# Performance work log

Hardware: AMD Instinct MI355X
Metric: run time of the kernel (lower is better)

The kernel has to match this reference:

```python
import jax, jax.numpy as jnp
import numpy as np

B, S, D, H, E = 4, 1024, 1024, 16, 4
HD = D // H
EPS = 1e-5


def setup_inputs() -> dict:
    key = jax.random.key(0)
    ks = jax.random.split(key, 6)
    std = 0.02
    return {
        "hidden_states": jax.random.normal(ks[0], (B, S, D), dtype=jnp.float32),
        "Wr": jax.random.normal(ks[1], (D, E), dtype=jnp.float32) * std,
        "br": jnp.zeros((E,), jnp.float32),
        "ln_g": jnp.ones((E, D), jnp.float32),
        "ln_b": jnp.zeros((E, D), jnp.float32),
        "W_attn": jax.random.normal(ks[2], (E, D, 3 * D), dtype=jnp.float32) * std,
        "b_attn": jnp.zeros((E, 3 * D), jnp.float32),
        "W_proj": jax.random.normal(ks[3], (E, D, D), dtype=jnp.float32) * std,
        "b_proj": jnp.zeros((E, D), jnp.float32),
    }


def reference(hidden_states, Wr, br, ln_g, ln_b, W_attn, b_attn, W_proj, b_proj):
    b, s, d = hidden_states.shape
    x = hidden_states.reshape(b * s, d)  # [N, D]

    # naive softmax router over experts
    score = jax.nn.softmax(x @ Wr + br, axis=-1)  # [N, E]

    # LayerNorm stats are expert-independent; affine is per-expert
    mu = jnp.mean(x, axis=-1, keepdims=True)
    var = jnp.mean(jnp.square(x - mu), axis=-1, keepdims=True)
    xn = (x - mu) * jax.lax.rsqrt(var + EPS)  # [N, D]

    ln_out = xn[:, None, :] * ln_g[None] + ln_b[None]  # [N, E, D]
    qkv_all = jnp.einsum('ned,edf->nef', ln_out, W_attn) + b_attn  # [N, E, 3D]
    # weighted_qkv: scale each expert's qkv by its routing score, sum
    qkv = jnp.einsum('ne,nef->nf', score, qkv_all)  # [N, 3D]

    q, k, v = jnp.split(qkv.reshape(b, s, 3 * d), 3, axis=-1)
    def split_heads(t):
        return t.reshape(b, s, H, HD).transpose(0, 2, 1, 3)  # [B,H,S,hd]
    q, k, v = split_heads(q), split_heads(k), split_heads(v)

    scale = 1.0 / jnp.sqrt(jnp.asarray(HD, q.dtype))
    att = jnp.einsum('bhqd,bhkd->bhqk', q, k) * scale  # [B,H,S,S]
    causal = jnp.tril(jnp.ones((s, s), dtype=bool))
    att = jnp.where(causal[None, None], att, jnp.finfo(att.dtype).min)
    probs = jax.nn.softmax(att, axis=-1)
    ctx = jnp.einsum('bhqk,bhkd->bhqd', probs, v)  # [B,H,S,hd]
    ctx = ctx.transpose(0, 2, 1, 3).reshape(b * s, d)  # [N, D]

    proj_all = jnp.einsum('nd,edf->nef', ctx, W_proj) + b_proj  # [N, E, D]
    out = jnp.einsum('ne,nef->nf', score, proj_all).reshape(b, s, d)
    return out
```

## Files before the change

kernel.cpp:

```cpp
#include <hip/hip_runtime.h>
#include <stdint.h>

#define NB 4
#define SS 1024
#define DD 1024
#define EE 4
#define HH 16
#define HDD 64
#define NN (NB*SS)
#define KK2 (EE*DD)
#define FF1 (3*DD)

typedef __attribute__((ext_vector_type(4))) float f32x4;
typedef __attribute__((ext_vector_type(8))) _Float16 half8;
typedef __attribute__((ext_vector_type(4))) _Float16 half4;

static __device__ __forceinline__ f32x4 mfma16(half8 a, half8 b, f32x4 c){
  return __builtin_amdgcn_mfma_f32_16x16x32_f16(a, b, c, 0, 0, 0);
}

#define GLOAD_LDS16(gp, lp) __builtin_amdgcn_global_load_lds( \
    (const unsigned int __attribute__((address_space(1)))*)(uintptr_t)(gp), \
    (unsigned int __attribute__((address_space(3)))*)(uintptr_t)(lp), 16, 0, 0)

#define SBAR() do { asm volatile("" ::: "memory"); \
                    __builtin_amdgcn_s_barrier(); \
                    asm volatile("" ::: "memory"); } while(0)

__global__ __launch_bounds__(256) void prep_kernel(
    const float* __restrict__ x, const float* __restrict__ Wr,
    const float* __restrict__ br, float* __restrict__ score,
    float* __restrict__ ratios, _Float16* __restrict__ xnb)
{
  int n = blockIdx.x;
  int tid = threadIdx.x;
  float4 xv = ((const float4*)(x + (size_t)n*DD))[tid];
  float xa[4] = {xv.x, xv.y, xv.z, xv.w};
  float vals[6];
  vals[0] = xa[0]+xa[1]+xa[2]+xa[3];
  vals[1] = xa[0]*xa[0]+xa[1]*xa[1]+xa[2]*xa[2]+xa[3]*xa[3];
  vals[2] = vals[3] = vals[4] = vals[5] = 0.f;
  #pragma unroll
  for (int j = 0; j < 4; ++j){
    float4 w = ((const float4*)Wr)[tid*4 + j];
    vals[2] += xa[j]*w.x; vals[3] += xa[j]*w.y;
    vals[4] += xa[j]*w.z; vals[5] += xa[j]*w.w;
  }
  #pragma unroll
  for (int off = 32; off >= 1; off >>= 1)
    #pragma unroll
    for (int i = 0; i < 6; ++i)
      vals[i] += __shfl_xor(vals[i], off, 64);
  __shared__ float red[4][6];
  int wid = tid >> 6;
  if ((tid & 63) == 0){
    #pragma unroll
    for (int i = 0; i < 6; ++i) red[wid][i] = vals[i];
  }
  __syncthreads();
  float tot[6];
  #pragma unroll
  for (int i = 0; i < 6; ++i)
    tot[i] = red[0][i] + red[1][i] + red[2][i] + red[3][i];

  float mu   = tot[0] * (1.f/DD);
  float var  = tot[1] * (1.f/DD) - mu*mu;
  float rsig = rsqrtf(var + 1e-5f);
  float lg[4];
  #pragma unroll
  for (int e = 0; e < 4; ++e) lg[e] = tot[2+e] + br[e];
  float mx = fmaxf(fmaxf(lg[0], lg[1]), fmaxf(lg[2], lg[3]));
  float ex[4], esum = 0.f;
  #pragma unroll
  for (int e = 0; e < 4; ++e){ ex[e] = __expf(lg[e] - mx); esum += ex[e]; }
  if (tid < 4){
    score[n*4 + tid] = ex[tid] / esum;
    ratios[n*4 + tid] = (tid > 0) ? (ex[tid-1] / ex[tid]) : 0.f;
  }

  half4 o;
  #pragma unroll
  for (int j = 0; j < 4; ++j) o[j] = (_Float16)((xa[j] - mu) * rsig);
  *(half4*)(xnb + (size_t)n*DD + tid*4) = o;
}

template<bool AFFINE>
__global__ __launch_bounds__(256) void transpose_f16_kernel(
    const float* __restrict__ W, _Float16* __restrict__ WT, int K, int F,
    const float* __restrict__ gvec, const float* __restrict__ bvec,
    float* __restrict__ part)
{
  __shared__ float t[64][65];
  __shared__ float red2[16][64];
  int k0 = blockIdx.x * 64, f0 = blockIdx.y * 64;
  int tid = threadIdx.x;
  int r = tid >> 4, c4 = (tid & 15) * 4;
  float pf[4] = {0.f, 0.f, 0.f, 0.f};
  #pragma unroll
  for (int i = 0; i < 4; ++i){
    int k = k0 + i*16 + r;
    float4 v = *(const float4*)(W + (size_t)k*F + f0 + c4);
    if constexpr (AFFINE){
      float bk = bvec[k];
      pf[0] += bk*v.x; pf[1] += bk*v.y; pf[2] += bk*v.z; pf[3] += bk*v.w;
      float gk = gvec[k];
      v.x *= gk; v.y *= gk; v.z *= gk; v.w *= gk;
    }
    t[i*16 + r][c4+0] = v.x; t[i*16 + r][c4+1] = v.y;
    t[i*16 + r][c4+2] = v.z; t[i*16 + r][c4+3] = v.w;
  }
  if constexpr (AFFINE){
    #pragma unroll
    for (int j = 0; j < 4; ++j) red2[r][c4+j] = pf[j];
  }
  __syncthreads();
  int f = tid >> 2, seg = tid & 3;
  half8 o0, o1;
  #pragma unroll
  for (int j = 0; j < 8; ++j){
    o0[j] = (_Float16)t[seg*16 + j][f];
    o1[j] = (_Float16)t[seg*16 + 8 + j][f];
  }
  _Float16* dst = WT + (size_t)(f0 + f)*K + k0 + seg*16;
  *(half8*)dst = o0;
  *(half8*)(dst + 8) = o1;
  if constexpr (AFFINE){
    if (tid < 64){
      float s = 0.f;
      #pragma unroll
      for (int rr = 0; rr < 16; ++rr) s += red2[rr][tid];
      part[(size_t)blockIdx.x * F + f0 + tid] = s;
    }
  }
}

__global__ __launch_bounds__(256) void bb1_kernel(
    const float* __restrict__ b_attn, const float* __restrict__ part,
    float* __restrict__ BB1)
{
  int idx = blockIdx.x*256 + threadIdx.x;
  int e = idx / FF1, f = idx - e*FF1;
  float s = b_attn[idx];
  #pragma unroll
  for (int i = 0; i < 16; ++i)
    s += part[(size_t)(e*16 + i)*FF1 + f];
  BB1[idx] = s;
}

#define G1_BM 256
#define G1_BN 192
#define G1_BK 64
#define G1_T  (KK2/G1_BK)
#define G1_ABUF (G1_BM*G1_BK)
#define G1_BBUF (G1_BN*G1_BK)
#define G1_BUFSZ (G1_ABUF+G1_BBUF)

__global__ __launch_bounds__(512, 2) void gemm1_kernel(
    const _Float16* __restrict__ XN, const _Float16* __restrict__ BT,
    const float* __restrict__ score, const float* __restrict__ ratios,
    const float* __restrict__ bias, _Float16* __restrict__ C)
{
  __shared__ _Float16 smem[2*G1_BUFSZ];
  int tid = threadIdx.x;
  int lane = tid & 63, wid = tid >> 6;
  int q = lane & 15, g = lane >> 4;
  int wr = wid >> 1, wc = wid & 1;
  int xo = (q & 7) << 3;
  int bid = blockIdx.x;
  int xcd = bid & 7, li = bid >> 3;
  int m0 = (li >> 1) * G1_BM;
  int n0 = (xcd*2 + (li & 1)) * G1_BN;

  int arow[4], brow[6];
  #pragma unroll
  for (int mf = 0; mf < 4; ++mf) arow[mf] = (wr*64 + mf*16 + q)*64;
  #pragma unroll
  for (int nf = 0; nf < 6; ++nf) brow[nf] = G1_ABUF + (wc*96 + nf*16 + q)*64;
  int soff[2] = { (g*8) ^ xo, (32 + g*8) ^ xo };

  auto stageA = [&](int t, int buf, int h){
    const int d0 = (t & 15) * G1_BK;
    _Float16* sA = smem + buf*G1_BUFSZ;
    #pragma unroll
    for (int ld = 0; ld < 2; ++ld){
      int l = h*2 + ld;
      int c = l*512 + tid;
      int row = c >> 3;
      int seg = (c & 7) ^ (row & 7);
      GLOAD_LDS16(XN + (size_t)(m0 + row)*DD + d0 + seg*8,
                  sA + (l*512 + wid*64)*8);
    }
  };
  auto stageB = [&](int t, int buf){
    const int k0 = t * G1_BK;
    _Float16* sB = smem + buf*G1_BUFSZ + G1_ABUF;
    #pragma unroll
    for (int ld = 0; ld < 3; ++ld){
      int c = ld*512 + tid;
      int row = c >> 3;
      int seg = (c & 7) ^ (row & 7);
      GLOAD_LDS16(BT + (size_t)(n0 + row)*KK2 + k0 + seg*8,
                  sB + (ld*512 + wid*64)*8);
    }
  };

  f32x4 acc[4][6] = {};
  half8 af0[2][2], af2[2][2], bfA[3][2], bfB[3][2];

  auto C1 = [&](){
    __builtin_amdgcn_s_setprio(1);
    #pragma unroll
    for (int k = 0; k < 2; ++k)
      #pragma unroll
      for (int m = 0; m < 2; ++m)
        #pragma unroll
        for (int n = 0; n < 3; ++n)
          acc[m][n] = mfma16(af0[m][k], bfA[n][k], acc[m][n]);
    __builtin_amdgcn_s_setprio(0);
  };
  auto C2 = [&](){
    __builtin_amdgcn_s_setprio(1);
    #pragma unroll
    for (int k = 0; k < 2; ++k)
      #pragma unroll
      for (int m = 0; m < 2; ++m)
        #pragma unroll
        for (int n = 0; n < 3; ++n)
          acc[2+m][n] = mfma16(af2[m][k], bfA[n][k], acc[2+m][n]);
    __builtin_amdgcn_s_setprio(0);
  };
  auto C3 = [&](){
    __builtin_amdgcn_s_setprio(1);
    #pragma unroll
    for (int k = 0; k < 2; ++k)
      #pragma unroll
      for (int m = 0; m < 2; ++m)
        #pragma unroll
        for (int n = 0; n < 3; ++n)
          acc[m][3+n] = mfma16(af0[m][k], bfB[n][k], acc[m][3+n]);
    __builtin_amdgcn_s_setprio(0);
  };
  auto C4 = [&](){
    __builtin_amdgcn_s_setprio(1);
    #pragma unroll
    for (int k = 0; k < 2; ++k)
      #pragma unroll
      for (int m = 0; m < 2; ++m)
        #pragma unroll
        for (int n = 0; n < 3; ++n)
          acc[2+m][3+n] = mfma16(af2[m][k], bfB[n][k], acc[2+m][3+n]);
    __builtin_amdgcn_s_setprio(0);
  };

  stageA(0, 0, 0); stageA(0, 0, 1); stageB(0, 0);

  for (int t = 0; t < G1_T-1; ++t){
    int buf = t & 1, nxt = buf ^ 1;
    const _Float16* base = smem + buf*G1_BUFSZ;
    stageA(t+1, nxt, 0);
    asm volatile("s_waitcnt vmcnt(2)" ::: "memory");
    SBAR();
    #pragma unroll
    for (int m = 0; m < 2; ++m)
      #pragma unroll
      for (int k = 0; k < 2; ++k)
        af0[m][k] = *(const half8*)(base + arow[m] + soff[k]);
    #pragma unroll
    for (int n = 0; n < 3; ++n)
      #pragma unroll
      for (int k = 0; k < 2; ++k)
        bfA[n][k] = *(const half8*)(base + brow[n] + soff[k]);
    if (t) C4();
    if (t && (t & 15) == 0){
      int e = t >> 4;
      #pragma unroll
      for (int mf = 0; mf < 4; ++mf)
        #pragma unroll
        for (int r = 0; r < 4; ++r){
          int gm = m0 + wr*64 + mf*16 + g*4 + r;
          float ratio = ratios[gm*4 + e];
          #pragma unroll
          for (int nf = 0; nf < 6; ++nf)
            acc[mf][nf][r] *= ratio;
        }
    }
    C1();
    stageA(t+1, nxt, 1);
    #pragma unroll
    for (int m = 0; m < 2; ++m)
      #pragma unroll
      for (int k = 0; k < 2; ++k)
        af2[m][k] = *(const half8*)(base + arow[2+m] + soff[k]);
    C2();
    stageB(t+1, nxt);
    #pragma unroll
    for (int n = 0; n < 3; ++n)
      #pragma unroll
      for (int k = 0; k < 2; ++k)
        bfB[n][k] = *(const half8*)(base + brow[3+n] + soff[k]);
    SBAR();
    C3();
  }
  {
    const _Float16* base = smem + ((G1_T-1) & 1)*G1_BUFSZ;
    asm volatile("s_waitcnt vmcnt(0)" ::: "memory");
    SBAR();
    C4();
    #pragma unroll
    for (int m = 0; m < 2; ++m)
      #pragma unroll
      for (int k = 0; k < 2; ++k){
        af0[m][k] = *(const half8*)(base + arow[m] + soff[k]);
        af2[m][k] = *(const half8*)(base + arow[2+m] + soff[k]);
      }
    #pragma unroll
    for (int n = 0; n < 3; ++n)
      #pragma unroll
      for (int k = 0; k < 2; ++k){
        bfA[n][k] = *(const half8*)(base + brow[n] + soff[k]);
        bfB[n][k] = *(const half8*)(base + brow[3+n] + soff[k]);
      }
    C1(); C2(); C3(); C4();
  }

  float bv[6][4];
  #pragma unroll
  for (int nf = 0; nf < 6; ++nf){
    int gn = n0 + wc*96 + nf*16 + q;
    #pragma unroll
    for (int e = 0; e < 4; ++e) bv[nf][e] = bias[e*FF1 + gn];
  }
  #pragma unroll
  for (int mf = 0; mf < 4; ++mf){
    #pragma unroll
    for (int r = 0; r < 4; ++r){
      int gm = m0 + wr*64 + mf*16 + g*4 + r;
      float4 sc = *(const float4*)(score + gm*4);
      #pragma unroll
      for (int nf = 0; nf < 6; ++nf){
        int gn = n0 + wc*96 + nf*16 + q;
        float v = acc[mf][nf][r]*sc.w
                + sc.x*bv[nf][0] + sc.y*bv[nf][1] + sc.z*bv[nf][2] + sc.w*bv[nf][3];
        C[(size_t)gm*FF1 + gn] = (_Float16)v;
      }
    }
  }
}

#define G2_BK 64
#define G2_ABUF (128*G2_BK)
#define G2_BUFSZ (2*G2_ABUF)

__global__ __launch_bounds__(512) void gemm2_kernel(
    const _Float16* __restrict__ CTX, const _Float16* __restrict__ BT,
    const float* __restrict__ score, const float* __restrict__ bias,
    float* __restrict__ Cout)
{
  __shared__ _Float16 smem[2*G2_BUFSZ];
  int tid = threadIdx.x;
  int lane = tid & 63, wid = tid >> 6;
  int q = lane & 15, g = lane >> 4;
  int wr = wid >> 2, wc = wid & 3;
  int xo = (q & 7) << 3;
  int bid = blockIdx.x;
  int xcd = bid >> 5, idx = bid & 31;
  int m0 = (xcd*4 + (idx >> 3)) * 128;
  int n0 = (idx & 7) * 128;

  int arow[4], brow[2];
  #pragma unroll
  for (int mf = 0; mf < 4; ++mf) arow[mf] = (wr*64 + mf*16 + q)*64;
  #pragma unroll
  for (int nf = 0; nf < 2; ++nf) brow[nf] = G2_ABUF + (wc*32 + nf*16 + q)*64;
  int soff[2] = { (g*8) ^ xo, (32 + g*8) ^ xo };

  auto stage = [&](int t, int buf){
    const int d0 = (t & 15) * G2_BK;
    const int k0 = t * G2_BK;
    _Float16* sA = smem + buf*G2_BUFSZ;
    _Float16* sB = sA + G2_ABUF;
    #pragma unroll
    for (int ld = 0; ld < 2; ++ld){
      int c = ld*512 + tid;
      int row = c >> 3;
      int seg = (c & 7) ^ (row & 7);
      GLOAD_LDS16(CTX + (size_t)(m0 + row)*DD + d0 + seg*8,
                  sA + (ld*512 + wid*64)*8);
    }
    #pragma unroll
    for (int ld = 0; ld < 2; ++ld){
      int c = ld*512 + tid;
      int row = c >> 3;
      int seg = (c & 7) ^ (row & 7);
      GLOAD_LDS16(BT + (size_t)(n0 + row)*KK2 + k0 + seg*8,
                  sB + (ld*512 + wid*64)*8);
    }
  };

  f32x4 accp[4][2] = {}, acco[4][2] = {};

  auto merge = [&](int e){
    #pragma unroll
    for (int m = 0; m < 4; ++m)
      #pragma unroll
      for (int r = 0; r < 4; ++r){
        int gm = m0 + wr*64 + m*16 + g*4 + r;
        float s = score[(size_t)gm*4 + e];
        #pragma unroll
        for (int n = 0; n < 2; ++n){
          acco[m][n][r] += s*accp[m][n][r];
          accp[m][n][r] = 0.f;
        }
      }
  };

  half8 af[4][2], bfr[2][2];
  auto reads = [&](const _Float16* base, int k){
    #pragma unroll
    for (int m = 0; m < 4; ++m)
      af[m][k] = *(const half8*)(base + arow[m] + soff[k]);
    #pragma unroll
    for (int n = 0; n < 2; ++n)
      bfr[n][k] = *(const half8*)(base + brow[n] + soff[k]);
  };
  auto mfmas = [&](int k){
    __builtin_amdgcn_s_setprio(1);
    #pragma unroll
    for (int m = 0; m < 4; ++m)
      #pragma unroll
      for (int n = 0; n < 2; ++n)
        accp[m][n] = mfma16(af[m][k], bfr[n][k], accp[m][n]);
    __builtin_amdgcn_s_setprio(0);
  };

  stage(0, 0);
  for (int t = 0; t < KK2/G2_BK - 1; ++t){
    const _Float16* base = smem + (t & 1)*G2_BUFSZ;
    stage(t+1, (t+1)&1);
    asm volatile("s_waitcnt vmcnt(4)" ::: "memory");
    SBAR();
    reads(base, 0);
    if (t) mfmas(1);
    if (t && (t & 15) == 0) merge((t >> 4) - 1);
    mfmas(0);
    reads(base, 1);
    SBAR();
  }
  {
    const _Float16* base = smem + ((KK2/G2_BK - 1) & 1)*G2_BUFSZ;
    asm volatile("s_waitcnt vmcnt(0)" ::: "memory");
    SBAR();
    mfmas(1);
    reads(base, 0); reads(base, 1);
    mfmas(0); mfmas(1);
    merge(3);
  }

  #pragma unroll
  for (int m = 0; m < 4; ++m){
    #pragma unroll
    for (int r = 0; r < 4; ++r){
      int gm = m0 + wr*64 + m*16 + g*4 + r;
      float4 sc = *(const float4*)(score + gm*4);
      #pragma unroll
      for (int n = 0; n < 2; ++n){
        int gn = n0 + wc*32 + n*16 + q;
        float v = acco[m][n][r]
                + sc.x*bias[gn] + sc.y*bias[DD+gn]
                + sc.z*bias[2*DD+gn] + sc.w*bias[3*DD+gn];
        Cout[(size_t)gm*DD + gn] = v;
      }
    }
  }
}

__global__ __launch_bounds__(512) void attn_kernel(
    const _Float16* __restrict__ qkv, _Float16* __restrict__ ctx)
{
  __shared__ _Float16 lsK[2][64*64];
  __shared__ _Float16 lsV[2][64*64];
  __shared__ _Float16 lsP[8][16*64];
  int bh = blockIdx.x, qt = blockIdx.y;
  int b = bh >> 4, h = bh & 15;
  int tid = threadIdx.x, lane = tid & 63, wid = tid >> 6;
  int q = lane & 15, g = lane >> 4;
  int xo = (q & 7) << 3;
  int qrow0 = qt*128 + wid*16;

  half8 qf[2];
  #pragma unroll
  for (int kk = 0; kk < 2; ++kk)
    qf[kk] = *(const half8*)(qkv + ((size_t)b*SS + qrow0 + q)*FF1 + h*HDD + kk*32 + g*8);

  auto issueK = [&](int kt, int buf){
    size_t kvrow = (size_t)b*SS + kt*64;
    int row = tid >> 3, seg = (tid & 7) ^ (row & 7);
    GLOAD_LDS16(qkv + (kvrow + row)*FF1 + DD + h*HDD + seg*8,
                lsK[buf] + (size_t)(wid*64)*8);
  };
  auto issueV = [&](int kt, half8& vr){
    size_t kvrow = (size_t)b*SS + kt*64;
    vr = *(const half8*)(qkv + (kvrow + lane)*FF1 + 2*DD + h*HDD + wid*8);
  };
  auto writeV = [&](half8 vr, int buf){
    #pragma unroll
    for (int j = 0; j < 8; ++j){
      int hd = wid*8 + j;
      lsV[buf][hd*64 + (lane ^ ((hd & 7) << 3))] = vr[j];
    }
  };

  f32x4 o[4] = {};
  float mrow = -1e30f, lsum = 0.f;
  const float SC2 = 0.18033688011112042f;
  int qglob = qrow0 + q;
  int ktmax = 2*qt + 1;

  half8 vr;
  issueK(0, 0);
  issueV(0, vr);

  for (int kt = 0; kt <= ktmax; ++kt){
    int cur = kt & 1, nxt = cur ^ 1;
    int tn = (kt < ktmax) ? kt+1 : ktmax;
    asm volatile("s_waitcnt vmcnt(1)" ::: "memory");
    SBAR();

    f32x4 st[4] = {};
    __builtin_amdgcn_s_setprio(1);
    #pragma unroll
    for (int i = 0; i < 4; ++i){
      #pragma unroll
      for (int kk = 0; kk < 2; ++kk){
        half8 kf = *(const half8*)(lsK[cur] + (i*16 + q)*64 + ((kk*32 + g*8) ^ xo));
        st[i] = mfma16(kf, qf[kk], st[i]);
      }
    }
    __builtin_amdgcn_s_setprio(0);
    issueK(tn, nxt);
    asm volatile("s_waitcnt vmcnt(1)" ::: "memory");
    writeV(vr, cur);

    float pvv[16]; float tm = -1e30f;
    if (kt*64 + 63 > qrow0){
      #pragma unroll
      for (int i = 0; i < 4; ++i)
        #pragma unroll
        for (int r = 0; r < 4; ++r){
          int kglob = kt*64 + i*16 + g*4 + r;
          float sv = (kglob <= qglob) ? st[i][r]*SC2 : -1e30f;
          pvv[i*4+r] = sv; tm = fmaxf(tm, sv);
        }
    } else {
      #pragma unroll
      for (int i = 0; i < 4; ++i)
        #pragma unroll
        for (int r = 0; r < 4; ++r){
          float sv = st[i][r]*SC2;
          pvv[i*4+r] = sv; tm = fmaxf(tm, sv);
        }
    }
    tm = fmaxf(tm, __shfl_xor(tm, 16, 64));
    tm = fmaxf(tm, __shfl_xor(tm, 32, 64));
    bool resc = !__all(tm <= mrow);
    float mnew = resc ? fmaxf(mrow, tm) : mrow;
    float psum = 0.f;
    _Float16 pb[16];
    #pragma unroll
    for (int i = 0; i < 16; ++i){
      float p = exp2f(pvv[i] - mnew);
      psum += p; pb[i] = (_Float16)p;
    }
    if (resc){
      float alpha = exp2f(mrow - mnew);
      mrow = mnew;
      lsum = lsum*alpha + psum;
      float af4[4];
      #pragma unroll
      for (int r = 0; r < 4; ++r) af4[r] = __shfl(alpha, g*4 + r, 64);
      #pragma unroll
      for (int n = 0; n < 4; ++n)
        #pragma unroll
        for (int r = 0; r < 4; ++r) o[n][r] *= af4[r];
    } else {
      lsum += psum;
    }
    issueV(tn, vr);

    asm volatile("s_waitcnt lgkmcnt(0)" ::: "memory");
    SBAR();

    #pragma unroll
    for (int i = 0; i < 4; ++i){
      half4 w4;
      w4[0]=pb[i*4+0]; w4[1]=pb[i*4+1]; w4[2]=pb[i*4+2]; w4[3]=pb[i*4+3];
      *(half4*)(&lsP[wid][q*64 + ((i*16 + g*4) ^ xo)]) = w4;
    }
    __builtin_amdgcn_s_setprio(1);
    #pragma unroll
    for (int kk = 0; kk < 2; ++kk){
      half8 pf = *(const half8*)(&lsP[wid][q*64 + ((kk*32 + g*8) ^ xo)]);
      #pragma unroll
      for (int n = 0; n < 4; ++n){
        half8 vf = *(const half8*)(&lsV[cur][(n*16 + q)*64 + ((kk*32 + g*8) ^ xo)]);
        o[n] = mfma16(pf, vf, o[n]);
      }
    }
    __builtin_amdgcn_s_setprio(0);
  }
  float lt = lsum + __shfl_xor(lsum, 16, 64);
  lt = lt + __shfl_xor(lt, 32, 64);
  float rinv = 1.f / lt;
  #pragma unroll
  for (int r = 0; r < 4; ++r){
    float ri = __shfl(rinv, g*4 + r, 64);
    int qg = qt*128 + wid*16 + g*4 + r;
    _Float16* obase = ctx + ((size_t)b*SS + qg)*DD + h*HDD;
    #pragma unroll
    for (int n = 0; n < 4; ++n)
      obase[n*16 + q] = (_Float16)(o[n][r] * ri);
  }
}

extern "C" void kernel_launch(void* const* d_in, const int* in_sizes, int n_in,
                              void* d_out, int out_size, void* d_ws, size_t ws_size,
                              hipStream_t stream)
{
  const float* x      = (const float*)d_in[0];
  const float* Wr     = (const float*)d_in[1];
  const float* br     = (const float*)d_in[2];
  const float* ln_g   = (const float*)d_in[3];
  const float* ln_b   = (const float*)d_in[4];
  const float* W_attn = (const float*)d_in[5];
  const float* b_attn = (const float*)d_in[6];
  const float* W_proj = (const float*)d_in[7];
  const float* b_proj = (const float*)d_in[8];
  (void)in_sizes; (void)n_in; (void)out_size; (void)ws_size;

  char* ws = (char*)d_ws;
  size_t off = 0;
  auto alloc = [&](size_t bytes) -> void* {
    void* p = ws + off; off += (bytes + 255) & ~(size_t)255; return p;
  };
  _Float16* W1gT  = (_Float16*)alloc((size_t)FF1*KK2*2);
  _Float16* W2T   = (_Float16*)alloc((size_t)DD*KK2*2);
  float*    score = (float*)   alloc((size_t)NN*4*4);
  float*    ratio = (float*)   alloc((size_t)NN*4*4);
  _Float16* xn16  = (_Float16*)alloc((size_t)NN*DD*2);
  _Float16* qkv   = (_Float16*)alloc((size_t)NN*FF1*2);
  _Float16* ctx   = (_Float16*)alloc((size_t)NN*DD*2);
  float*    part  = (float*)   alloc((size_t)(KK2/64)*FF1*4);
  float*    BB1   = (float*)   alloc((size_t)EE*FF1*4);

  hipLaunchKernelGGL((transpose_f16_kernel<true>), dim3(KK2/64, FF1/64), dim3(256), 0, stream,
                     W_attn, W1gT, KK2, FF1, ln_g, ln_b, part);
  hipLaunchKernelGGL((transpose_f16_kernel<false>), dim3(KK2/64, DD/64), dim3(256), 0, stream,
                     W_proj, W2T, KK2, DD, nullptr, nullptr, nullptr);
  hipLaunchKernelGGL(bb1_kernel, dim3(EE*FF1/256), dim3(256), 0, stream,
                     b_attn, part, BB1);
  hipLaunchKernelGGL(prep_kernel, dim3(NN), dim3(256), 0, stream,
                     x, Wr, br, score, ratio, xn16);
  hipLaunchKernelGGL(gemm1_kernel, dim3(256), dim3(512), 0, stream,
                     xn16, W1gT, score, ratio, BB1, qkv);
  hipLaunchKernelGGL(attn_kernel, dim3(NB*HH, SS/128), dim3(512), 0, stream,
                     qkv, ctx);
  hipLaunchKernelGGL(gemm2_kernel, dim3(256), dim3(512), 0, stream,
                     ctx, W2T, score, b_proj, (float*)d_out);
}
```

Before: 200.7 us.

## Load GEMM1 A operand directly from global into registers, stage only B in LDS

The A operand (normalized activations) of the first GEMM is no longer staged through LDS; each wave loads its MFMA fragments directly from global memory into registers, double-buffered across iterations. LDS now holds only the B tiles, and the block-to-tile mapping is swapped so M follows the XCD index. The aim is to cut LDS footprint and LDS traffic for A, which is reused across the four experts' K-slices. In exchange, each wave issues uncoalesced 16-byte global loads per row, and the wait becomes a full vmcnt(0) with a simpler, less interleaved MFMA schedule.

```diff
diff --git a/kernel.cpp b/kernel.cpp
--- a/kernel.cpp
+++ b/kernel.cpp
@@ -151,16 +151,14 @@
 #define G1_BN 192
 #define G1_BK 64
 #define G1_T  (KK2/G1_BK)
-#define G1_ABUF (G1_BM*G1_BK)
 #define G1_BBUF (G1_BN*G1_BK)
-#define G1_BUFSZ (G1_ABUF+G1_BBUF)
 
 __global__ __launch_bounds__(512, 2) void gemm1_kernel(
     const _Float16* __restrict__ XN, const _Float16* __restrict__ BT,
     const float* __restrict__ score, const float* __restrict__ ratios,
     const float* __restrict__ bias, _Float16* __restrict__ C)
 {
-  __shared__ _Float16 smem[2*G1_BUFSZ];
+  __shared__ _Float16 smem[2*G1_BBUF];
   int tid = threadIdx.x;
   int lane = tid & 63, wid = tid >> 6;
   int q = lane & 15, g = lane >> 4;
@@ -168,32 +166,22 @@
   int xo = (q & 7) << 3;
   int bid = blockIdx.x;
   int xcd = bid & 7, li = bid >> 3;
-  int m0 = (li >> 1) * G1_BM;
-  int n0 = (xcd*2 + (li & 1)) * G1_BN;
-
-  int arow[4], brow[6];
-  #pragma unroll
-  for (int mf = 0; mf < 4; ++mf) arow[mf] = (wr*64 + mf*16 + q)*64;
-  #pragma unroll
-  for (int nf = 0; nf < 6; ++nf) brow[nf] = G1_ABUF + (wc*96 + nf*16 + q)*64;
+  int m0 = (xcd*2 + (li & 1)) * G1_BM;
+  int n0 = (li >> 1) * G1_BN;
+
+  const _Float16* aptr[4];
+  #pragma unroll
+  for (int mf = 0; mf < 4; ++mf)
+    aptr[mf] = XN + (size_t)(m0 + wr*64 + mf*16 + q)*DD + g*8;
+
+  int brow[6];
+  #pragma unroll
+  for (int nf = 0; nf < 6; ++nf) brow[nf] = (wc*96 + nf*16 + q)*64;
   int soff[2] = { (g*8) ^ xo, (32 + g*8) ^ xo };
 
-  auto stageA = [&](int t, int buf, int h){
-    const int d0 = (t & 15) * G1_BK;
-    _Float16* sA = smem + buf*G1_BUFSZ;
-    #pragma unroll
-    for (int ld = 0; ld < 2; ++ld){
-      int l = h*2 + ld;
-      int c = l*512 + tid;
-      int row = c >> 3;
-      int seg = (c & 7) ^ (row & 7);
-      GLOAD_LDS16(XN + (size_t)(m0 + row)*DD + d0 + seg*8,
-                  sA + (l*512 + wid*64)*8);
-    }
-  };
   auto stageB = [&](int t, int buf){
     const int k0 = t * G1_BK;
-    _Float16* sB = smem + buf*G1_BUFSZ + G1_ABUF;
+    _Float16* sB = smem + buf*G1_BBUF;
     #pragma unroll
     for (int ld = 0; ld < 3; ++ld){
       int c = ld*512 + tid;
@@ -203,74 +191,26 @@
                   sB + (ld*512 + wid*64)*8);
     }
   };
+  auto loadA = [&](int t, half8 (&ar)[4][2]){
+    const int d0 = (t & 15) * G1_BK;
+    #pragma unroll
+    for (int mf = 0; mf < 4; ++mf)
+      #pragma unroll
+      for (int k = 0; k < 2; ++k)
+        ar[mf][k] = *(const half8*)(aptr[mf] + d0 + k*32);
+  };
 
   f32x4 acc[4][6] = {};
-  half8 af0[2][2], af2[2][2], bfA[3][2], bfB[3][2];
-
-  auto C1 = [&](){
-    __builtin_amdgcn_s_setprio(1);
-    #pragma unroll
-    for (int k = 0; k < 2; ++k)
-      #pragma unroll
-      for (int m = 0; m < 2; ++m)
-        #pragma unroll
-        for (int n = 0; n < 3; ++n)
-          acc[m][n] = mfma16(af0[m][k], bfA[n][k], acc[m][n]);
-    __builtin_amdgcn_s_setprio(0);
-  };
-  auto C2 = [&](){
-    __builtin_amdgcn_s_setprio(1);
-    #pragma unroll
-    for (int k = 0; k < 2; ++k)
-      #pragma unroll
-      for (int m = 0; m < 2; ++m)
-        #pragma unroll
-        for (int n = 0; n < 3; ++n)
-          acc[2+m][n] = mfma16(af2[m][k], bfA[n][k], acc[2+m][n]);
-    __builtin_amdgcn_s_setprio(0);
-  };
-  auto C3 = [&](){
-    __builtin_amdgcn_s_setprio(1);
-    #pragma unroll
-    for (int k = 0; k < 2; ++k)
-      #pragma unroll
-      for (int m = 0; m < 2; ++m)
-        #pragma unroll
-        for (int n = 0; n < 3; ++n)
-          acc[m][3+n] = mfma16(af0[m][k], bfB[n][k], acc[m][3+n]);
-    __builtin_amdgcn_s_setprio(0);
-  };
-  auto C4 = [&](){
-    __builtin_amdgcn_s_setprio(1);
-    #pragma unroll
-    for (int k = 0; k < 2; ++k)
-      #pragma unroll
-      for (int m = 0; m < 2; ++m)
-        #pragma unroll
-        for (int n = 0; n < 3; ++n)
-          acc[2+m][3+n] = mfma16(af2[m][k], bfB[n][k], acc[2+m][3+n]);
-    __builtin_amdgcn_s_setprio(0);
-  };
-
-  stageA(0, 0, 0); stageA(0, 0, 1); stageB(0, 0);
-
-  for (int t = 0; t < G1_T-1; ++t){
-    int buf = t & 1, nxt = buf ^ 1;
-    const _Float16* base = smem + buf*G1_BUFSZ;
-    stageA(t+1, nxt, 0);
-    asm volatile("s_waitcnt vmcnt(2)" ::: "memory");
+  half8 aA[4][2], aB[4][2];
+
+  loadA(0, aA); stageB(0, 0);
+
+  auto body = [&](int t, half8 (&aCur)[4][2], half8 (&aNxt)[4][2]){
+    int buf = t & 1;
+    const _Float16* base = smem + buf*G1_BBUF;
+    asm volatile("s_waitcnt vmcnt(0)" ::: "memory");
     SBAR();
-    #pragma unroll
-    for (int m = 0; m < 2; ++m)
-      #pragma unroll
-      for (int k = 0; k < 2; ++k)
-        af0[m][k] = *(const half8*)(base + arow[m] + soff[k]);
-    #pragma unroll
-    for (int n = 0; n < 3; ++n)
-      #pragma unroll
-      for (int k = 0; k < 2; ++k)
-        bfA[n][k] = *(const half8*)(base + brow[n] + soff[k]);
-    if (t) C4();
+    if (t < G1_T-1){ loadA(t+1, aNxt); stageB(t+1, buf^1); }
     if (t && (t & 15) == 0){
       int e = t >> 4;
       #pragma unroll
@@ -284,43 +224,53 @@
             acc[mf][nf][r] *= ratio;
         }
     }
-    C1();
-    stageA(t+1, nxt, 1);
-    #pragma unroll
-    for (int m = 0; m < 2; ++m)
+    half8 bfA[3][2], bfB[3][2];
+    #pragma unroll
+    for (int n = 0; n < 3; ++n)
       #pragma unroll
       for (int k = 0; k < 2; ++k)
-        af2[m][k] = *(const half8*)(base + arow[2+m] + soff[k]);
-    C2();
-    stageB(t+1, nxt);
+        bfA[n][k] = *(const half8*)(base + brow[n] + soff[k]);
     #pragma unroll
     for (int n = 0; n < 3; ++n)
       #pragma unroll
       for (int k = 0; k < 2; ++k)
         bfB[n][k] = *(const half8*)(base + brow[3+n] + soff[k]);
-    SBAR();
-    C3();
-  }
-  {
-    const _Float16* base = smem + ((G1_T-1) & 1)*G1_BUFSZ;
-    asm volatile("s_waitcnt vmcnt(0)" ::: "memory");
-    SBAR();
-    C4();
-    #pragma unroll
-    for (int m = 0; m < 2; ++m)
-      #pragma unroll
-      for (int k = 0; k < 2; ++k){
-        af0[m][k] = *(const half8*)(base + arow[m] + soff[k]);
-        af2[m][k] = *(const half8*)(base + arow[2+m] + soff[k]);
-      }
-    #pragma unroll
-    for (int n = 0; n < 3; ++n)
-      #pragma unroll
-      for (int k = 0; k < 2; ++k){
-        bfA[n][k] = *(const half8*)(base + brow[n] + soff[k]);
-        bfB[n][k] = *(const half8*)(base + brow[3+n] + soff[k]);
-      }
-    C1(); C2(); C3(); C4();
+    __builtin_amdgcn_s_setprio(1);
+    #pragma unroll
+    for (int k = 0; k < 2; ++k)
+      #pragma unroll
+      for (int m = 0; m < 2; ++m)
+        #pragma unroll
+        for (int n = 0; n < 3; ++n)
+          acc[m][n] = mfma16(aCur[m][k], bfA[n][k], acc[m][n]);
+    #pragma unroll
+    for (int k = 0; k < 2; ++k)
+      #pragma unroll
+      for (int m = 0; m < 2; ++m)
+        #pragma unroll
+        for (int n = 0; n < 3; ++n)
+          acc[2+m][n] = mfma16(aCur[2+m][k], bfA[n][k], acc[2+m][n]);
+    #pragma unroll
+    for (int k = 0; k < 2; ++k)
+      #pragma unroll
+      for (int m = 0; m < 2; ++m)
+        #pragma unroll
+        for (int n = 0; n < 3; ++n)
+          acc[m][3+n] = mfma16(aCur[m][k], bfB[n][k], acc[m][3+n]);
+    #pragma unroll
+    for (int k = 0; k < 2; ++k)
+      #pragma unroll
+      for (int m = 0; m < 2; ++m)
+        #pragma unroll
+        for (int n = 0; n < 3; ++n)
+          acc[2+m][3+n] = mfma16(aCur[2+m][k], bfB[n][k], acc[2+m][3+n]);
+    __builtin_amdgcn_s_setprio(0);
+  };
+
+  #pragma unroll 1
+  for (int t = 0; t < G1_T; t += 2){
+    body(t,   aA, aB);
+    body(t+1, aB, aA);
   }
 
   float bv[6][4];
```

Result: slower. 274.6 us (+36.8%).
